# Optimization experiments

Measured on AMD Instinct MI355X. Metric: run time of the kernel, lower is better.

The kernel has to match this reference:

```python
import jax, jax.numpy as jnp
import numpy as np

B, N, M = 8, 1024, 64          # graphs, ops/graph, machines/graph
OPF, MF = 16, 8                # raw feature dims
H, D, L = 8, 64, 3             # heads, head dim, HGT layers
F = H * D                      # 512 = hidden_dim * num_heads
KC = 8                         # compatible machines per op
NOP, NM = B * N, B * M
EPS = 1e-5


def _graph_ln(x, w, b):
    # PyG LayerNorm(mode='graph') with batch=None: scalar mean/std over the whole tensor
    x = x - x.mean()
    return x / (x.std() + EPS) * w + b


def _seg_softmax(a, idx, n):
    amax = jax.ops.segment_max(a, idx, num_segments=n)
    amax = jnp.where(jnp.isfinite(amax), amax, 0.0)
    ex = jnp.exp(a - amax[idx])
    s = jax.ops.segment_sum(ex, idx, num_segments=n)
    return ex / (s[idx] + 1e-16)


def _forward(op_x, machine_x, W_emb_op, b_emb_op, W_emb_m, b_emb_m,
             opn_w, opn_b, mn_w, mn_b, Wk, bk, Wq, bq, Wv, bv,
             A_rel, M_rel, p_rel, W_out, b_out, skip, ln_w, ln_b,
             ei_precedes, ei_canproc, ei_compat):
    x_op = _graph_ln(op_x @ W_emb_op + b_emb_op, opn_w, opn_b)
    x_m = _graph_ln(machine_x @ W_emb_m + b_emb_m, mn_w, mn_b)
    s0, d0 = ei_precedes   # op -> op
    s1, d1 = ei_canproc    # machine -> op
    s2, d2 = ei_compat     # op -> machine
    scale = 1.0 / jnp.sqrt(jnp.float32(D))
    for l in range(L):
        k_op = (x_op @ Wk[l, 0] + bk[l, 0]).reshape(NOP, H, D)
        q_op = (x_op @ Wq[l, 0] + bq[l, 0]).reshape(NOP, H, D)
        v_op = (x_op @ Wv[l, 0] + bv[l, 0]).reshape(NOP, H, D)
        k_m = (x_m @ Wk[l, 1] + bk[l, 1]).reshape(NM, H, D)
        q_m = (x_m @ Wq[l, 1] + bq[l, 1]).reshape(NM, H, D)
        v_m = (x_m @ Wv[l, 1] + bv[l, 1]).reshape(NM, H, D)
        # relation-specific per-head transforms (a_rel/m_rel of HGTConv)
        k0 = jnp.einsum('nhd,hde->nhe', k_op, A_rel[l, 0]); v0 = jnp.einsum('nhd,hde->nhe', v_op, M_rel[l, 0])
        k1 = jnp.einsum('nhd,hde->nhe', k_m, A_rel[l, 1]);  v1 = jnp.einsum('nhd,hde->nhe', v_m, M_rel[l, 1])
        k2 = jnp.einsum('nhd,hde->nhe', k_op, A_rel[l, 2]); v2 = jnp.einsum('nhd,hde->nhe', v_op, M_rel[l, 2])
        # attention into op nodes: joint softmax over both incoming edge types
        a0 = (q_op[d0] * k0[s0]).sum(-1) * p_rel[l, 0] * scale   # [E0,H]
        a1 = (q_op[d1] * k1[s1]).sum(-1) * p_rel[l, 1] * scale   # [E1,H]
        a_op = jnp.concatenate([a0, a1]); dd = jnp.concatenate([d0, d1])
        w = _seg_softmax(a_op, dd, NOP)
        msg = jnp.concatenate([v0[s0], v1[s1]]) * w[:, :, None]
        agg_op = jax.ops.segment_sum(msg, dd, num_segments=NOP).reshape(NOP, F)
        # attention into machine nodes
        a2 = (q_m[d2] * k2[s2]).sum(-1) * p_rel[l, 2] * scale
        w2 = _seg_softmax(a2, d2, NM)
        agg_m = jax.ops.segment_sum(v2[s2] * w2[:, :, None], d2, num_segments=NM).reshape(NM, F)
        # output projection + learned skip gate (HGTConv internals)
        o_op = jax.nn.gelu(agg_op, approximate=False) @ W_out[l, 0] + b_out[l, 0]
        o_m = jax.nn.gelu(agg_m, approximate=False) @ W_out[l, 1] + b_out[l, 1]
        g_op = jax.nn.sigmoid(skip[l, 0]); g_m = jax.nn.sigmoid(skip[l, 1])
        o_op = g_op * o_op + (1.0 - g_op) * x_op
        o_m = g_m * o_m + (1.0 - g_m) * x_m
        # wrapper residual + dropout(eval=identity) + graph layer norm
        x_op = _graph_ln(o_op + x_op, ln_w[l], ln_b[l])
        x_m = _graph_ln(o_m + x_m, ln_w[l], ln_b[l])
    fea_j = x_op.reshape(B, N, F)
    fea_m = x_m.reshape(B, M, F)
    return fea_j, fea_m, fea_j.mean(1, keepdims=True), fea_m.mean(1, keepdims=True)


def setup_inputs() -> dict:
    key = jax.random.key(0)
    ks = jax.random.split(key, 12)
    rng = np.random.default_rng(0)
    ids = np.arange(NOP).reshape(B, N)
    src0 = ids[:, :-1].ravel(); dst0 = ids[:, 1:].ravel()
    mach = rng.integers(0, M, size=(B, N, KC)) + (np.arange(B) * M)[:, None, None]
    ops = np.broadcast_to(ids[:, :, None], (B, N, KC))
    ei_precedes = jnp.asarray(np.stack([src0, dst0]), dtype=jnp.int32)
    ei_canproc = jnp.asarray(np.stack([mach.ravel(), ops.ravel()]), dtype=jnp.int32)
    ei_compat = jnp.asarray(np.stack([ops.ravel(), mach.ravel()]), dtype=jnp.int32)
    n = lambda k, sh, s=0.05: jax.random.normal(k, sh, dtype=jnp.float32) * s
    return dict(
        op_x=n(ks[0], (NOP, OPF), 1.0),
        machine_x=n(ks[1], (NM, MF), 1.0),
        W_emb_op=n(ks[2], (OPF, F)), b_emb_op=jnp.zeros((F,), jnp.float32),
        W_emb_m=n(ks[3], (MF, F)), b_emb_m=jnp.zeros((F,), jnp.float32),
        opn_w=jnp.ones((F,), jnp.float32), opn_b=jnp.zeros((F,), jnp.float32),
        mn_w=jnp.ones((F,), jnp.float32), mn_b=jnp.zeros((F,), jnp.float32),
        Wk=n(ks[4], (L, 2, F, F)), bk=jnp.zeros((L, 2, F), jnp.float32),
        Wq=n(ks[5], (L, 2, F, F)), bq=jnp.zeros((L, 2, F), jnp.float32),
        Wv=n(ks[6], (L, 2, F, F)), bv=jnp.zeros((L, 2, F), jnp.float32),
        A_rel=n(ks[7], (L, 3, H, D, D)), M_rel=n(ks[8], (L, 3, H, D, D)),
        p_rel=jnp.ones((L, 3, H), jnp.float32),
        W_out=n(ks[9], (L, 2, F, F)), b_out=jnp.zeros((L, 2, F), jnp.float32),
        skip=jnp.ones((L, 2), jnp.float32),
        ln_w=jnp.ones((L, F), jnp.float32), ln_b=jnp.zeros((L, F), jnp.float32),
        ei_precedes=ei_precedes, ei_canproc=ei_canproc, ei_compat=ei_compat,
    )


def reference(op_x, machine_x, W_emb_op, b_emb_op, W_emb_m, b_emb_m,
              opn_w, opn_b, mn_w, mn_b, Wk, bk, Wq, bq, Wv, bv,
              A_rel, M_rel, p_rel, W_out, b_out, skip, ln_w, ln_b,
              ei_precedes, ei_canproc, ei_compat):
    return _forward(op_x, machine_x, W_emb_op, b_emb_op, W_emb_m, b_emb_m,
                    opn_w, opn_b, mn_w, mn_b, Wk, bk, Wq, bq, Wv, bv,
                    A_rel, M_rel, p_rel, W_out, b_out, skip, ln_w, ln_b,
                    ei_precedes, ei_canproc, ei_compat)
```

## Files before the change

kernel.cpp:

```cpp
#include <hip/hip_runtime.h>

typedef unsigned short u16;
typedef __attribute__((ext_vector_type(4))) float floatx4;
typedef __attribute__((ext_vector_type(8))) short shortx8;
typedef __attribute__((ext_vector_type(4))) short shortx4;

#define NOPS 8192
#define NMS  512
#define CQ   2560
#define CM   1536
#define TOPC (NOPS*512)
#define TMC  (NMS*512)

__device__ __forceinline__ float bf2f(u16 u){ return __uint_as_float(((unsigned)u)<<16); }
__device__ __forceinline__ u16 f2bf(float f){
  unsigned u = __float_as_uint(f);
  u += 0x7FFFu + ((u>>16)&1u);
  return (u16)(u>>16);
}
__device__ __forceinline__ float wred(float v){
  #pragma unroll
  for (int o=32;o;o>>=1) v += __shfl_xor(v,o,64);
  return v;
}
__device__ __forceinline__ float geluf(float x){
  return 0.5f*x*(1.f+erff(x*0.70710678118654752f));
}
__device__ __forceinline__ void block_stat_out2(float s, float s2, float* pstat, int slot){
  __shared__ float sb[8];
  s = wred(s); s2 = wred(s2);
  int wv = threadIdx.x >> 6;
  if ((threadIdx.x & 63) == 0){ sb[wv*2] = s; sb[wv*2+1] = s2; }
  __syncthreads();
  if (threadIdx.x == 0){
    float a = 0.f, b = 0.f;
    int nw = blockDim.x >> 6;
    for (int i=0;i<nw;++i){ a += sb[i*2]; b += sb[i*2+1]; }
    pstat[slot*2]   = a;
    pstat[slot*2+1] = b;
  }
}

__global__ __launch_bounds__(256) void setup_all_k(
    const int* __restrict__ s1, float* __restrict__ Ct, float* __restrict__ Cn,
    const float* __restrict__ bq, float* bias_op, float* bias_m,
    const float* __restrict__ bk, const float* __restrict__ bv,
    const float* __restrict__ Ar, const float* __restrict__ Mr,
    const float* __restrict__ Wout, const float* __restrict__ Wq,
    u16* __restrict__ Wout_t, u16* __restrict__ Wc_op_t, u16* __restrict__ Wc_m_t,
    const float* __restrict__ Wk, const float* __restrict__ Wv,
    const float* __restrict__ Xop, const float* __restrict__ Wop, const float* __restrict__ bop,
    float* __restrict__ Yop, u16* __restrict__ Yop_bf,
    const float* __restrict__ Xm, const float* __restrict__ Wm, const float* __restrict__ bm_,
    float* __restrict__ Ym, u16* __restrict__ Ym_bf,
    float* pstat, float* pstat_m){
  __shared__ __align__(16) char smem[27648];
  int bid = blockIdx.x;
  int tid = threadIdx.x;
  if (bid < 2048){
    int idx = bid*256 + tid;
    int n = idx >> 6, l = idx & 63;
    const int* row = s1 + n*8;
    int cnt = 0;
    #pragma unroll
    for (int j=0;j<8;++j) cnt += ((row[j] & 63) == l);
    float f = (float)cnt;
    Cn[(size_t)n*64 + l] = f;
    int b = n >> 10, nl = n & 1023;
    Ct[(size_t)((b<<6) + l)*1024 + nl] = f;
  } else if (bid < 2060){
    int i = (bid-2048)*256 + tid;
    int l = i >> 10, side = (i >> 9) & 1, f = i & 511;
    float v = bq[(l*2+side)*512 + f];
    if (side==0) bias_op[l*CQ + f] = v; else bias_m[l*CM + f] = v;
  } else if (bid < 2204){
    if (tid >= 64) return;
    int gx = bid - 2060; int e = tid;
    int l = gx/48; int rem = gx - l*48; int s = rem >> 3; int h = rem & 7;
    int side = (s < 4) ? 0 : 1;
    int r = (s < 4) ? (s+1) : (s-3);
    int useK = side==0 ? (s==0 || s==2) : (s==4);
    int rel  = side==0 ? ((s<2)?0:2) : 1;
    const float* bb  = (useK ? bk : bv) + (size_t)(l*2+side)*512 + h*64;
    const float* Rel = (useK ? Ar : Mr) + ((size_t)(l*3+rel)*8 + h)*4096;
    float acc = 0.f;
    for (int d=0; d<64; ++d) acc += bb[d]*Rel[d*64 + e];
    float* bias = side ? (bias_m + l*CM) : (bias_op + l*CQ);
    bias[r*512 + h*64 + e] = acc;
  } else if (bid < 2972){
    u16 (*t)[65] = (u16(*)[65])smem;
    int id2 = bid - 2204;
    int g = id2 >> 6; int rem = id2 & 63;
    int kb = (rem >> 3) * 64, nb = (rem & 7) * 64;
    const float* s; u16* d;
    if (g < 6){
      s = Wout + (size_t)g*262144;
      d = Wout_t + (size_t)g*262144;
    } else {
      int blk = g - 6; int l = blk >> 1, side = blk & 1;
      s = Wq + (size_t)blk*262144;
      d = side ? (Wc_m_t + (size_t)l*CM*512) : (Wc_op_t + (size_t)l*CQ*512);
    }
    int tx = tid & 63, ty4 = tid >> 6;
    #pragma unroll 4
    for (int p=0;p<16;++p){
      int k = ty4 + p*4;
      t[k][tx] = f2bf(s[(size_t)(kb+k)*512 + nb + tx]);
    }
    __syncthreads();
    #pragma unroll 4
    for (int p=0;p<16;++p){
      int n = ty4 + p*4;
      d[(size_t)(nb+n)*512 + kb + tx] = t[tx][n];
    }
  } else if (bid < 3548){
    u16* As = (u16*)smem;
    u16* Bs = As + 64*72;
    int id3 = bid - 2972;
    int gx = id3 >> 2;
    int cc0 = (id3 & 3) * 128;
    int l = gx/48; int rem = gx - l*48; int s = rem >> 3; int h = rem & 7;
    int side = (s < 4) ? 0 : 1;
    int r = (s < 4) ? (s+1) : (s-3);
    int useK = side==0 ? (s==0 || s==2) : (s==4);
    int rel  = side==0 ? ((s<2)?0:2) : 1;
    const float* W   = (useK ? Wk : Wv) + (size_t)(l*2+side)*262144;
    const float* Rel = (useK ? Ar : Mr) + ((size_t)(l*3+rel)*8 + h)*4096;
    int h64 = h*64;
    u16* Wt = side ? (Wc_m_t + (size_t)l*CM*512) : (Wc_op_t + (size_t)l*CQ*512);
    int rbase = r*512 + h64;
    int lane = tid & 63, wave = tid >> 6;
    {
      int d = tid >> 2, e0 = (tid & 3) * 16;
      #pragma unroll
      for (int j=0;j<16;++j) As[(e0+j)*72 + d] = f2bf(Rel[d*64 + e0 + j]);
    }
    {
      int ccl = tid >> 1, d0 = (tid & 1) * 32;
      const float* src = W + (size_t)(cc0+ccl)*512 + h64 + d0;
      #pragma unroll
      for (int j=0;j<32;j+=4){
        floatx4 v = *(const floatx4*)(src + j);
        shortx4 sv;
        #pragma unroll
        for (int e=0;e<4;++e) sv[e] = (short)f2bf(v[e]);
        *(shortx4*)(Bs + ccl*72 + d0 + j) = sv;
      }
    }
    __syncthreads();
    int wm = wave & 1, wn = wave >> 1;
    int mrow = lane & 15, quad = lane >> 4;
    floatx4 acc[2][4];
    #pragma unroll
    for (int a=0;a<2;++a)
      #pragma unroll
      for (int b=0;b<4;++b) acc[a][b] = (floatx4){0.f,0.f,0.f,0.f};
    #pragma unroll
    for (int ks=0; ks<2; ++ks){
      shortx8 af[2], bf[4];
      #pragma unroll
      for (int mt=0;mt<2;++mt) af[mt] = *(const shortx8*)(As + (wm*32 + mt*16 + mrow)*72 + ks*32 + quad*8);
      #pragma unroll
      for (int nt=0;nt<4;++nt) bf[nt] = *(const shortx8*)(Bs + (wn*64 + nt*16 + mrow)*72 + ks*32 + quad*8);
      #pragma unroll
      for (int mt=0;mt<2;++mt)
        #pragma unroll
        for (int nt=0;nt<4;++nt)
          acc[mt][nt] = __builtin_amdgcn_mfma_f32_16x16x32_bf16(af[mt], bf[nt], acc[mt][nt], 0, 0, 0);
    }
    #pragma unroll
    for (int mt=0;mt<2;++mt){
      #pragma unroll
      for (int nt=0;nt<4;++nt){
        int ccl = wn*64 + nt*16 + mrow;
        #pragma unroll
        for (int r2=0;r2<4;++r2){
          int e = wm*32 + mt*16 + quad*4 + r2;
          Wt[(size_t)(rbase + e)*512 + cc0 + ccl] = f2bf(acc[mt][nt][r2]);
        }
      }
    }
  } else {
    int eb = bid - 3548;
    const float *X, *W, *bias; float *Y, *ps; u16* Yb; int K, total, nb, lb;
    if (eb < 1024){ X=Xop; W=Wop; bias=bop; Y=Yop; Yb=Yop_bf; ps=pstat;   K=16; total=TOPC; nb=1024; lb=eb; }
    else          { X=Xm;  W=Wm;  bias=bm_; Y=Ym;  Yb=Ym_bf;  ps=pstat_m; K=8;  total=TMC;  nb=128;  lb=eb-1024; }
    float s = 0.f, s2 = 0.f;
    for (int idx = lb*256 + tid; idx < total; idx += nb*256){
      int n = idx >> 9, f = idx & 511;
      float v = bias[f];
      for (int c=0;c<K;++c) v += X[n*K+c] * W[c*512+f];
      Y[idx] = v;
      Yb[idx] = f2bf(v);
      s += v; s2 += v*v;
    }
    block_stat_out2(s, s2, ps, lb);
  }
}

__global__ __launch_bounds__(256) void foldk(u16* __restrict__ Wc_op_t, u16* __restrict__ Wc_m_t,
                                             float* __restrict__ bias_op, float* __restrict__ bias_m,
                                             float* __restrict__ u_op, float* __restrict__ u_m,
                                             const float* __restrict__ opn_w, const float* __restrict__ opn_b,
                                             const float* __restrict__ mn_w, const float* __restrict__ mn_b,
                                             const float* __restrict__ ln_w, const float* __restrict__ ln_b){
  int bid = blockIdx.x, tid = threadIdx.x;
  int rloc = tid >> 2, t = tid & 3;
  int side, l; u16* Wt; float* bias; float* u;
  if (bid < 120){
    int row = bid*64 + rloc; side = 0; l = row/2560; int j = row - l*2560;
    Wt = Wc_op_t + ((size_t)l*CQ + j)*512; bias = bias_op + l*CQ + j; u = u_op + l*CQ + j;
  } else {
    int row = (bid-120)*64 + rloc; side = 1; l = row/1536; int j = row - l*1536;
    Wt = Wc_m_t + ((size_t)l*CM + j)*512; bias = bias_m + l*CM + j; u = u_m + l*CM + j;
  }
  const float* w = side ? (l==0 ? mn_w : ln_w + (l-1)*512) : (l==0 ? opn_w : ln_w + (l-1)*512);
  const float* b = side ? (l==0 ? mn_b : ln_b + (l-1)*512) : (l==0 ? opn_b : ln_b + (l-1)*512);
  float up = 0.f, vp = 0.f;
  for (int k = t*128; k < t*128 + 128; k += 8){
    shortx8 wv = *(shortx8*)(Wt + k);
    #pragma unroll
    for (int e=0;e<8;++e){
      float x = bf2f((u16)wv[e]);
      float wk = w[k+e];
      up += wk*x; vp += b[k+e]*x;
      wv[e] = (short)f2bf(x*wk);
    }
    *(shortx8*)(Wt + k) = wv;
  }
  up += __shfl_xor(up,1,64); up += __shfl_xor(up,2,64);
  vp += __shfl_xor(vp,1,64); vp += __shfl_xor(vp,2,64);
  if (t == 0){ *u = up; *bias += vp; }
}

__global__ __launch_bounds__(256) void ln2_k(const float* __restrict__ src_op, float* __restrict__ dst_op,
                                             const float* __restrict__ w_op, const float* __restrict__ b_op,
                                             const float* __restrict__ src_m, float* __restrict__ dst_m,
                                             const float* __restrict__ w_m, const float* __restrict__ b_m,
                                             const float* __restrict__ pstat, const float* __restrict__ pstat_m,
                                             int nbo, int nbm){
  int bid = blockIdx.x;
  const float *src, *w, *b, *ps; float* dst; int total4, nb, lb, nblk; float inv_n;
  if (bid < 1024){ src=src_op; dst=dst_op; w=w_op; b=b_op; ps=pstat;
                   total4=TOPC/4; nb=1024; lb=bid; nblk=nbo; inv_n=1.f/TOPC; }
  else           { src=src_m;  dst=dst_m;  w=w_m;  b=b_m;  ps=pstat_m;
                   total4=TMC/4;  nb=128;  lb=bid-1024; nblk=nbm; inv_n=1.f/TMC; }
  __shared__ float sb[8];
  __shared__ float mr[2];
  float s = 0.f, s2 = 0.f;
  for (int i = threadIdx.x; i < nblk; i += 256){ s += ps[2*i]; s2 += ps[2*i+1]; }
  s = wred(s); s2 = wred(s2);
  int wv = threadIdx.x >> 6;
  if ((threadIdx.x & 63) == 0){ sb[wv*2] = s; sb[wv*2+1] = s2; }
  __syncthreads();
  if (threadIdx.x == 0){
    float a = 0.f, bsum = 0.f;
    for (int i=0;i<4;++i){ a += sb[i*2]; bsum += sb[i*2+1]; }
    float mean = a * inv_n;
    float var  = fmaxf(bsum * inv_n - mean*mean, 0.f);
    mr[0] = mean;
    mr[1] = 1.f/(sqrtf(var) + 1e-5f);
  }
  __syncthreads();
  float mean = mr[0], rinv = mr[1];
  const floatx4* s4 = (const floatx4*)src;
  floatx4* d4 = (floatx4*)dst;
  const floatx4* w4 = (const floatx4*)w;
  const floatx4* b4 = (const floatx4*)b;
  for (int i = lb*256 + threadIdx.x; i < total4; i += nb*256){
    int f = i & 127;
    floatx4 v = s4[i], wv2 = w4[f], bv = b4[f];
    #pragma unroll
    for (int e=0;e<4;++e) v[e] = (v[e]-mean)*rinv*wv2[e] + bv[e];
    d4[i] = v;
  }
}

__device__ __forceinline__ void gemm_gate_core(u16* As, u16* Bs, float* stb,
                                               const u16* __restrict__ A, const u16* __restrict__ Bt,
                                               const float* __restrict__ xr, const float* __restrict__ bo,
                                               const float* __restrict__ sk,
                                               const float* __restrict__ lnw, const float* __restrict__ lnb,
                                               const float* __restrict__ psr, int np, float inv_n,
                                               float* __restrict__ Y, u16* __restrict__ Ybf,
                                               float* pstat, int slot, int bx, int by){
  const int tid = threadIdx.x;
  const int lane = tid & 63, wave = tid >> 6;
  {
    float s = 0.f, s2 = 0.f;
    for (int i = tid; i < np; i += 256){ s += psr[2*i]; s2 += psr[2*i+1]; }
    s = wred(s); s2 = wred(s2);
    if (lane == 0){ stb[wave*2] = s; stb[wave*2+1] = s2; }
    __syncthreads();
    if (tid == 0){
      float a = 0.f, bb = 0.f;
      for (int i=0;i<4;++i){ a += stb[2*i]; bb += stb[2*i+1]; }
      float mean = a * inv_n;
      float var = fmaxf(bb * inv_n - mean*mean, 0.f);
      stb[8] = mean;
      stb[9] = 1.f/(sqrtf(var) + 1e-5f);
    }
    __syncthreads();
  }
  const float mean = stb[8], rinv = stb[9];
  const int bm = by * 128, bn = bx * 128;
  const int wm = wave & 1, wn = wave >> 1;
  const int mrow = lane & 15, quad = lane >> 4;
  const u16* Ab = A + (size_t)bm*512;
  const u16* Bb = Bt + (size_t)bn*512;
  floatx4 acc[4][4];
  #pragma unroll
  for (int a=0;a<4;++a)
    #pragma unroll
    for (int b=0;b<4;++b) acc[a][b] = (floatx4){0.f,0.f,0.f,0.f};
  const int r0 = tid >> 2, c0 = (tid & 3) * 8;
  const int r1 = (tid+256) >> 2, c1 = ((tid+256) & 3) * 8;
  const int lds0 = wave*512;
  const int lds1 = wave*512 + 2048;
  for (int k0 = 0; k0 < 512; k0 += 32){
    __builtin_amdgcn_global_load_lds((const __attribute__((address_space(1))) void*)(Ab + (size_t)r0*512 + k0 + c0),
                                     (__attribute__((address_space(3))) void*)(As + lds0), 16, 0, 0);
    __builtin_amdgcn_global_load_lds((const __attribute__((address_space(1))) void*)(Ab + (size_t)r1*512 + k0 + c1),
                                     (__attribute__((address_space(3))) void*)(As + lds1), 16, 0, 0);
    __builtin_amdgcn_global_load_lds((const __attribute__((address_space(1))) void*)(Bb + (size_t)r0*512 + k0 + c0),
                                     (__attribute__((address_space(3))) void*)(Bs + lds0), 16, 0, 0);
    __builtin_amdgcn_global_load_lds((const __attribute__((address_space(1))) void*)(Bb + (size_t)r1*512 + k0 + c1),
                                     (__attribute__((address_space(3))) void*)(Bs + lds1), 16, 0, 0);
    __syncthreads();
    shortx8 af[4], bf[4];
    #pragma unroll
    for (int mt=0;mt<4;++mt) af[mt] = *(const shortx8*)(As + (wm*64 + mt*16 + mrow)*32 + quad*8);
    #pragma unroll
    for (int nt=0;nt<4;++nt) bf[nt] = *(const shortx8*)(Bs + (wn*64 + nt*16 + mrow)*32 + quad*8);
    #pragma unroll
    for (int mt=0;mt<4;++mt)
      #pragma unroll
      for (int nt=0;nt<4;++nt)
        acc[mt][nt] = __builtin_amdgcn_mfma_f32_16x16x32_bf16(af[mt], bf[nt], acc[mt][nt], 0, 0, 0);
    __syncthreads();
  }
  float g = 1.f/(1.f+expf(-(*sk)));
  float s = 0.f, s2 = 0.f;
  #pragma unroll
  for (int mt=0;mt<4;++mt){
    #pragma unroll
    for (int nt=0;nt<4;++nt){
      int col = bn + wn*64 + nt*16 + mrow;
      float bval = bo[col];
      float lw = lnw[col]*rinv, lb = lnb[col];
      #pragma unroll
      for (int r2=0;r2<4;++r2){
        int row = bm + wm*64 + mt*16 + quad*4 + r2;
        float v = acc[mt][nt][r2] + bval;
        float xv = (xr[(size_t)row*512 + col] - mean)*lw + lb;
        float o = g*v + (2.f-g)*xv;
        Y[(size_t)row*512 + col] = o;
        Ybf[(size_t)row*512 + col] = f2bf(o);
        s += o; s2 += o*o;
      }
    }
  }
  block_stat_out2(s, s2, pstat, slot);
}
__global__ __launch_bounds__(256) void gemmgate2_k(
    const u16* A1, const u16* B1, const float* x1, const float* bo1, const float* sk1,
    const float* lnw1, const float* lnb1, float* Y1, u16* Yb1, float* ps1w, int nblk1,
    const u16* A2, const u16* B2, const float* x2, const float* bo2, const float* sk2,
    const float* lnw2, const float* lnb2, float* Y2, u16* Yb2, float* ps2w,
    const float* ps1r, int np1, const float* ps2r, int np2){
  __shared__ u16 As[128*32];
  __shared__ u16 Bs[128*32];
  __shared__ float stb[12];
  int id = blockIdx.x;
  if (id < nblk1)
    gemm_gate_core(As, Bs, stb, A1, B1, x1, bo1, sk1, lnw1, lnb1, ps1r, np1, 1.f/TOPC,
                   Y1, Yb1, ps1w, id, id % 4, id / 4);
  else {
    int j = id - nblk1;
    gemm_gate_core(As, Bs, stb, A2, B2, x2, bo2, sk2, lnw2, lnb2, ps2r, np2, 1.f/TMC,
                   Y2, Yb2, ps2w, j, j % 4, j / 4);
  }
}

__device__ __forceinline__ void stage_half8(const u16* __restrict__ src, int kc, u16* region, int tid){
  int wave = tid >> 6;
  #pragma unroll
  for (int j=0;j<2;++j){
    int idx = j*512 + tid;
    int row = idx >> 2, qp2 = idx & 3;
    int qs = qp2 ^ (((row >> 3) & 1) << 1);
    __builtin_amdgcn_global_load_lds(
      (const __attribute__((address_space(1))) void*)(src + (size_t)row*512 + kc + qs*8),
      (__attribute__((address_space(3))) void*)(region + (j*512 + wave*64)*8),
      16, 0, 0);
  }
}

#define MFMA_QUAD(MH) do { \
  __builtin_amdgcn_s_barrier(); \
  asm volatile("s_waitcnt lgkmcnt(0)" ::: "memory"); \
  __builtin_amdgcn_sched_barrier(0); \
  __builtin_amdgcn_s_setprio(1); \
  _Pragma("unroll") \
  for (int mt=0;mt<4;++mt){ \
    _Pragma("unroll") \
    for (int nt=0;nt<4;++nt) \
      acc[(MH)*4+mt][nt] = __builtin_amdgcn_mfma_f32_16x16x32_bf16(af[mt], bf[nt], acc[(MH)*4+mt][nt], 0, 0, 0); \
  } \
  __builtin_amdgcn_s_setprio(0); \
} while(0)

__global__ __launch_bounds__(512, 2) void gemm8_k(
    const u16* __restrict__ A1, const u16* __restrict__ B1, const float* __restrict__ bias1,
    const float* __restrict__ u1, u16* __restrict__ C1, int N1, int nbx1, int nblk1,
    const u16* __restrict__ A2, const u16* __restrict__ B2, const float* __restrict__ bias2p,
    const float* __restrict__ u2, u16* __restrict__ C2, int N2, int nbx2,
    const float* __restrict__ ps1, int np1, const float* __restrict__ ps2, int np2){
  extern __shared__ u16 lds[];
  float* statsh = (float*)(lds + 65536);
  int id = blockIdx.x;
  const u16 *A, *Bt; const float *bias, *uvec, *ps; u16* C; int N, bx, by, np; float inv_n;
  if (id < nblk1){
    int xcd = id & 7, loc = id >> 3;
    int wg = xcd * (nblk1 >> 3) + loc;
    A=A1; Bt=B1; bias=bias1; uvec=u1; C=C1; N=N1; bx=wg%nbx1; by=wg/nbx1;
    ps=ps1; np=np1; inv_n=1.f/TOPC;
  }
  else { int j=id-nblk1; A=A2; Bt=B2; bias=bias2p; uvec=u2; C=C2; N=N2; bx=j%nbx2; by=j/nbx2;
    ps=ps2; np=np2; inv_n=1.f/TMC; }
  const int tid = threadIdx.x, lane = tid & 63, wave = tid >> 6;
  {
    float s = 0.f, s2 = 0.f;
    for (int i = tid; i < np; i += 512){ s += ps[2*i]; s2 += ps[2*i+1]; }
    s = wred(s); s2 = wred(s2);
    if (lane == 0){ statsh[wave*2] = s; statsh[wave*2+1] = s2; }
    __syncthreads();
    if (tid == 0){
      float a = 0.f, bb = 0.f;
      for (int i=0;i<8;++i){ a += statsh[2*i]; bb += statsh[2*i+1]; }
      float mean = a * inv_n;
      float var = fmaxf(bb * inv_n - mean*mean, 0.f);
      statsh[16] = mean;
      statsh[17] = 1.f/(sqrtf(var) + 1e-5f);
    }
    __syncthreads();
  }
  const float mean = statsh[16], rinv = statsh[17];
  const int wm = wave & 1, wn = wave >> 1;
  const int mrow = lane & 15, quad = lane >> 4;
  const int qp = quad ^ ((mrow & 8) ? 2 : 0);
  const u16* Ab = A + (size_t)(by*256)*512;
  const u16* Bb = Bt + (size_t)(bx*256)*512;

  floatx4 acc[8][4];
  #pragma unroll
  for (int a=0;a<8;++a)
    #pragma unroll
    for (int b=0;b<4;++b) acc[a][b] = (floatx4){0.f,0.f,0.f,0.f};

  stage_half8(Ab, 0,  lds,          tid);
  stage_half8(Bb, 0,  lds + 16384,  tid);
  stage_half8(Ab, 32, lds + 8192,   tid);
  stage_half8(Bb, 32, lds + 24576,  tid);
  stage_half8(Ab, 64, lds + 32768,  tid);
  stage_half8(Bb, 64, lds + 49152,  tid);
  asm volatile("s_waitcnt vmcnt(8)" ::: "memory");
  __builtin_amdgcn_s_barrier();

  for (int t = 0; t < 8; ++t){
    const int s = t & 1;
    u16* Sbase = lds + s*32768;
    u16* Obase = lds + (s^1)*32768;
    const u16* a0 = Sbase + (wm*128 + mrow)*32 + qp*8;
    const u16* b0 = Sbase + 16384 + (wn*64 + mrow)*32 + qp*8;
    const int kc1 = ((t < 7) ? (t+1) : 7)*64 + 32;
    const int kc2 = ((t < 6) ? (t+2) : 7)*64;
    shortx8 af[4], bf[4];

    #pragma unroll
    for (int mt=0;mt<4;++mt) af[mt] = *(const shortx8*)(a0 + mt*512);
    #pragma unroll
    for (int nt=0;nt<4;++nt) bf[nt] = *(const shortx8*)(b0 + nt*512);
    stage_half8(Ab, kc1, Obase + 8192, tid);
    MFMA_QUAD(0);
    __builtin_amdgcn_s_barrier();

    #pragma unroll
    for (int mt=0;mt<4;++mt) af[mt] = *(const shortx8*)(a0 + 2048 + mt*512);
    stage_half8(Bb, kc1, Obase + 24576, tid);
    MFMA_QUAD(1);
    asm volatile("s_waitcnt vmcnt(8)" ::: "memory");
    __builtin_amdgcn_s_barrier();

    #pragma unroll
    for (int mt=0;mt<4;++mt) af[mt] = *(const shortx8*)(a0 + 8192 + mt*512);
    #pragma unroll
    for (int nt=0;nt<4;++nt) bf[nt] = *(const shortx8*)(b0 + 8192 + nt*512);
    stage_half8(Ab, kc2, Sbase, tid);
    MFMA_QUAD(0);
    __builtin_amdgcn_s_barrier();

    #pragma unroll
    for (int mt=0;mt<4;++mt) af[mt] = *(const shortx8*)(a0 + 8192 + 2048 + mt*512);
    stage_half8(Bb, kc2, Sbase + 16384, tid);
    MFMA_QUAD(1);
    asm volatile("s_waitcnt vmcnt(8)" ::: "memory");
    __builtin_amdgcn_s_barrier();
  }

  const float rm = rinv*mean;
  const int crow0 = by*256 + wm*128 + quad*4;
  const int ccol0 = bx*256 + wn*64 + mrow;
  float bv[4], uv[4];
  #pragma unroll
  for (int nt=0;nt<4;++nt){
    int col = ccol0 + nt*16;
    bv[nt] = bias[col];
    uv[nt] = uvec[col];
  }
  #pragma unroll
  for (int mh=0;mh<2;++mh){
    #pragma unroll
    for (int mt=0;mt<4;++mt){
      int row = crow0 + mh*64 + mt*16;
      #pragma unroll
      for (int nt=0;nt<4;++nt){
        int col = ccol0 + nt*16;
        #pragma unroll
        for (int r2=0;r2<4;++r2)
          C[(size_t)(row+r2)*N + col] = f2bf(rinv*acc[mh*4+mt][nt][r2] + bv[nt] - rm*uv[nt]);
      }
    }
  }
}

__global__ __launch_bounds__(256) void attn_k(const u16* __restrict__ qkv_op, const u16* __restrict__ qkv_m,
                                              const float* __restrict__ prel, const float* __restrict__ Cn,
                                              const float* __restrict__ Ct,
                                              u16* __restrict__ agg_op, u16* __restrict__ agg_m){
  __shared__ __align__(16) char smem[43520];
  int id = blockIdx.x;
  int tid = threadIdx.x, lane = tid & 63, wave = tid >> 6;
  int mrow = lane & 15, quad = lane >> 4;
  if (id < 1024){
    u16* smem16 = (u16*)smem;
    u16* As = smem16;
    u16* Bs = smem16 + 4608;
    float* Sbuf = (float*)smem;
    u16* P   = smem16 + 9216;
    u16* v1T = smem16 + 13824;
    float* wpreS = (float*)(smem + 36864);
    float* linvS = (float*)(smem + 37120);
    int bh = id >> 4; int b = bh >> 3, h = bh & 7;
    int n0 = (id & 15) * 64;
    int wm = wave & 1, wn = wave >> 1;
    int srow = tid >> 2, scol = (tid & 3) * 16;
    float p1 = prel[8 + h] * 0.125f;
    {
      const u16* src = qkv_op + (size_t)(b*1024 + n0 + srow)*CQ + h*64 + scol;
      *(shortx8*)(As + srow*72 + scol)     = *(const shortx8*)(src);
      *(shortx8*)(As + srow*72 + scol + 8) = *(const shortx8*)(src + 8);
    }
    {
      const u16* src = qkv_m + (size_t)(b*64 + srow)*CM + 512 + h*64 + scol;
      *(shortx8*)(Bs + srow*72 + scol)     = *(const shortx8*)(src);
      *(shortx8*)(Bs + srow*72 + scol + 8) = *(const shortx8*)(src + 8);
    }
    {
      const u16* src = qkv_m + (size_t)(b*64 + srow)*CM + 1024 + h*64 + scol;
      shortx8 v0 = *(const shortx8*)(src);
      shortx8 v1 = *(const shortx8*)(src + 8);
      #pragma unroll
      for (int e=0;e<8;++e){ v1T[(scol+e)*72 + srow] = (u16)v0[e]; v1T[(scol+8+e)*72 + srow] = (u16)v1[e]; }
    }
    __syncthreads();
    floatx4 acc[2][2];
    #pragma unroll
    for (int a=0;a<2;++a){ acc[a][0] = (floatx4){0,0,0,0}; acc[a][1] = (floatx4){0,0,0,0}; }
    #pragma unroll
    for (int ks=0; ks<2; ++ks){
      shortx8 af[2], bf[2];
      #pragma unroll
      for (int mt=0;mt<2;++mt) af[mt] = *(const shortx8*)(As + (wm*32 + mt*16 + mrow)*72 + ks*32 + quad*8);
      #pragma unroll
      for (int nt=0;nt<2;++nt) bf[nt] = *(const shortx8*)(Bs + (wn*32 + nt*16 + mrow)*72 + ks*32 + quad*8);
      #pragma unroll
      for (int mt=0;mt<2;++mt)
        #pragma unroll
        for (int nt=0;nt<2;++nt)
          acc[mt][nt] = __builtin_amdgcn_mfma_f32_16x16x32_bf16(af[mt], bf[nt], acc[mt][nt], 0, 0, 0);
    }
    __syncthreads();
    #pragma unroll
    for (int mt=0;mt<2;++mt){
      #pragma unroll
      for (int nt=0;nt<2;++nt){
        int m = wn*32 + nt*16 + mrow;
        #pragma unroll
        for (int r2=0;r2<4;++r2){
          int nl = wm*32 + mt*16 + quad*4 + r2;
          Sbuf[nl*66 + m] = acc[mt][nt][r2] * p1;
        }
      }
    }
    __syncthreads();
    {
      int row = srow;
      int mb  = scol;
      int n_g = b*1024 + n0 + row;
      int nl  = n0 + row;
      float sp = -1e30f;
      if (nl > 0){
        float p0 = prel[h] * 0.125f;
        const u16* qp = qkv_op + (size_t)n_g*CQ + h*64 + mb;
        const u16* kp = qkv_op + (size_t)(n_g-1)*CQ + 512 + h*64 + mb;
        shortx8 qa = *(const shortx8*)(qp), qb2 = *(const shortx8*)(qp + 8);
        shortx8 ka = *(const shortx8*)(kp), kb2 = *(const shortx8*)(kp + 8);
        float d = 0.f;
        #pragma unroll
        for (int e=0;e<8;++e) d += bf2f((u16)qa[e])*bf2f((u16)ka[e]) + bf2f((u16)qb2[e])*bf2f((u16)kb2[e]);
        d += __shfl_xor(d, 1, 64);
        d += __shfl_xor(d, 2, 64);
        sp = d * p0;
      }
      const float* crow = Cn + (size_t)n_g*64 + mb;
      float cv[16];
      float mx = sp;
      #pragma unroll
      for (int j=0;j<16;++j){
        cv[j] = crow[j];
        if (cv[j] > 0.f) mx = fmaxf(mx, Sbuf[row*66 + mb + j]);
      }
      mx = fmaxf(mx, __shfl_xor(mx, 1, 64));
      mx = fmaxf(mx, __shfl_xor(mx, 2, 64));
      float L = 0.f;
      #pragma unroll
      for (int j=0;j<16;j+=4){
        shortx4 pv;
        #pragma unroll
        for (int e=0;e<4;++e){
          float w = (cv[j+e] > 0.f) ? cv[j+e]*expf(Sbuf[row*66 + mb + j + e] - mx) : 0.f;
          L += w;
          pv[e] = (short)f2bf(w);
        }
        *(shortx4*)(P + row*72 + mb + j) = pv;
      }
      L += __shfl_xor(L, 1, 64);
      L += __shfl_xor(L, 2, 64);
      float ep = (nl > 0) ? expf(sp - mx) : 0.f;
      L += ep;
      if ((tid & 3) == 0){ wpreS[row] = ep; linvS[row] = 1.f/(L + 1e-16f); }
    }
    __syncthreads();
    floatx4 po[2][2];
    #pragma unroll
    for (int a=0;a<2;++a){ po[a][0] = (floatx4){0,0,0,0}; po[a][1] = (floatx4){0,0,0,0}; }
    #pragma unroll
    for (int ks=0; ks<2; ++ks){
      shortx8 paf[2], pbf[2];
      #pragma unroll
      for (int mt=0;mt<2;++mt) paf[mt] = *(const shortx8*)(P + (wm*32 + mt*16 + mrow)*72 + ks*32 + quad*8);
      #pragma unroll
      for (int nt=0;nt<2;++nt) pbf[nt] = *(const shortx8*)(v1T + (wn*32 + nt*16 + mrow)*72 + ks*32 + quad*8);
      #pragma unroll
      for (int mt=0;mt<2;++mt)
        #pragma unroll
        for (int nt=0;nt<2;++nt)
          po[mt][nt] = __builtin_amdgcn_mfma_f32_16x16x32_bf16(paf[mt], pbf[nt], po[mt][nt], 0, 0, 0);
    }
    #pragma unroll
    for (int mt=0;mt<2;++mt){
      #pragma unroll
      for (int nt=0;nt<2;++nt){
        int d = wn*32 + nt*16 + mrow;
        #pragma unroll
        for (int r2=0;r2<4;++r2){
          int rl = wm*32 + mt*16 + quad*4 + r2;
          int n = n0 + rl;
          size_t ng = (size_t)b*1024 + n;
          float v = po[mt][nt][r2];
          if (n > 0) v += wpreS[rl] * bf2f(qkv_op[(ng-1)*CQ + 1024 + h*64 + d]);
          v *= linvS[rl];
          agg_op[ng*512 + h*64 + d] = f2bf(geluf(v));
        }
      }
    }
  } else {
    u16* qs  = (u16*)smem;
    u16* ks  = (u16*)(smem + 2304);
    u16* vsT = (u16*)(smem + 20736);
    u16* Ps  = (u16*)(smem + 38144);
    float (*redv)[4][16] = (float(*)[4][16])(smem + 42496);
    int id2 = id - 1024;
    int g = id2 & 3; int bh = id2 >> 2; int b = bh >> 3, h = bh & 7;
    int w = wave;
    float p2 = prel[16 + h] * 0.125f;
    if (tid < 128){
      int r = tid >> 3, cg = (tid & 7) * 8;
      *(shortx8*)(qs + r*72 + cg) = *(const shortx8*)(qkv_m + (size_t)(b*64 + g*16 + r)*CM + h*64 + cg);
    }
    const float* ctbase = Ct + (size_t)(b*64 + g*16 + mrow)*1024;
    float mx = -1e30f;
    for (int ch = 0; ch < 8; ++ch){
      int nb = ch*128;
      #pragma unroll
      for (int i=0;i<4;++i){
        int idx = i*256 + tid;
        int r = idx >> 3, cg = (idx & 7) * 8;
        *(shortx8*)(ks + r*72 + cg) =
          *(const shortx8*)(qkv_op + (size_t)(b*1024 + nb + r)*CQ + 1536 + h*64 + cg);
      }
      __syncthreads();
      #pragma unroll
      for (int nt=0; nt<2; ++nt){
        floatx4 acc = (floatx4){0,0,0,0};
        #pragma unroll
        for (int kk=0; kk<2; ++kk){
          shortx8 af = *(const shortx8*)(ks + (w*32 + nt*16 + mrow)*72 + kk*32 + quad*8);
          shortx8 bf = *(const shortx8*)(qs + mrow*72 + kk*32 + quad*8);
          acc = __builtin_amdgcn_mfma_f32_16x16x32_bf16(af, bf, acc, 0, 0, 0);
        }
        int nloc = w*32 + nt*16 + quad*4;
        floatx4 cv = *(const floatx4*)(ctbase + nb + nloc);
        #pragma unroll
        for (int r2=0;r2<4;++r2)
          if (cv[r2] > 0.f) mx = fmaxf(mx, acc[r2]*p2);
      }
      __syncthreads();
    }
    mx = fmaxf(mx, __shfl_xor(mx, 16, 64));
    mx = fmaxf(mx, __shfl_xor(mx, 32, 64));
    if (lane < 16) redv[0][w][lane] = mx;
    __syncthreads();
    mx = fmaxf(fmaxf(redv[0][0][mrow], redv[0][1][mrow]), fmaxf(redv[0][2][mrow], redv[0][3][mrow]));
    float L = 0.f;
    floatx4 O = (floatx4){0,0,0,0};
    for (int ch = 0; ch < 8; ++ch){
      int nb = ch*128;
      #pragma unroll
      for (int i=0;i<4;++i){
        int idx = i*256 + tid;
        int r = idx >> 3, cg = (idx & 7) * 8;
        *(shortx8*)(ks + r*72 + cg) =
          *(const shortx8*)(qkv_op + (size_t)(b*1024 + nb + r)*CQ + 1536 + h*64 + cg);
        shortx8 vv = *(const shortx8*)(qkv_op + (size_t)(b*1024 + nb + r)*CQ + 2048 + h*64 + cg);
        #pragma unroll
        for (int e=0;e<8;++e) vsT[(cg+e)*136 + r] = (u16)vv[e];
      }
      __syncthreads();
      #pragma unroll
      for (int nt=0; nt<2; ++nt){
        floatx4 acc = (floatx4){0,0,0,0};
        #pragma unroll
        for (int kk=0; kk<2; ++kk){
          shortx8 af = *(const shortx8*)(ks + (w*32 + nt*16 + mrow)*72 + kk*32 + quad*8);
          shortx8 bf = *(const shortx8*)(qs + mrow*72 + kk*32 + quad*8);
          acc = __builtin_amdgcn_mfma_f32_16x16x32_bf16(af, bf, acc, 0, 0, 0);
        }
        int nloc = w*32 + nt*16 + quad*4;
        floatx4 cv = *(const floatx4*)(ctbase + nb + nloc);
        shortx4 pv;
        #pragma unroll
        for (int r2=0;r2<4;++r2){
          float e = (cv[r2] > 0.f) ? cv[r2]*expf(acc[r2]*p2 - mx) : 0.f;
          L += e;
          pv[r2] = (short)f2bf(e);
        }
        *(shortx4*)(Ps + mrow*136 + nloc) = pv;
      }
      __syncthreads();
      #pragma unroll
      for (int kk=0; kk<4; ++kk){
        shortx8 af = *(const shortx8*)(Ps + mrow*136 + kk*32 + quad*8);
        shortx8 bf = *(const shortx8*)(vsT + (w*16 + mrow)*136 + kk*32 + quad*8);
        O = __builtin_amdgcn_mfma_f32_16x16x32_bf16(af, bf, O, 0, 0, 0);
      }
      __syncthreads();
    }
    L += __shfl_xor(L, 16, 64);
    L += __shfl_xor(L, 32, 64);
    if (lane < 16) redv[1][w][lane] = L;
    __syncthreads();
    #pragma unroll
    for (int r2=0;r2<4;++r2){
      int m = quad*4 + r2;
      float Ls = redv[1][0][m] + redv[1][1][m] + redv[1][2][m] + redv[1][3][m];
      float v = O[r2] / (Ls + 1e-16f);
      agg_m[(size_t)(b*64 + g*16 + m)*512 + h*64 + w*16 + mrow] = f2bf(geluf(v));
    }
  }
}

__global__ __launch_bounds__(512) void meanj_part_k(const float* __restrict__ xo, float* scratchJ){
  int b = blockIdx.x, chunk = blockIdx.y, f = threadIdx.x;
  float s = 0.f;
  for (int r=0;r<128;++r){
    int row = b*1024 + chunk*128 + r;
    s += xo[(size_t)row*512 + f];
  }
  scratchJ[(b*8 + chunk)*512 + f] = s;
}
__global__ __launch_bounds__(512) void mean2_k(const float* __restrict__ scratchJ, float* __restrict__ out){
  int i = blockIdx.x*512 + threadIdx.x;
  if (i < 4096){
    int b = i >> 9, f = i & 511;
    float s = 0.f;
    #pragma unroll
    for (int c=0;c<8;++c) s += scratchJ[(b*8+c)*512 + f];
    out[4456448 + i] = s * (1.f/1024.f);
  } else {
    int j = i - 4096;
    int b = j >> 9, f = j & 511;
    float s = 0.f;
    for (int r=0;r<64;++r) s += out[(size_t)TOPC + (size_t)(b*64+r)*512 + f];
    out[4460544 + j] = s * (1.f/64.f);
  }
}

extern "C" void kernel_launch(void* const* d_in, const int* in_sizes, int n_in,
                              void* d_out, int out_size, void* d_ws, size_t ws_size,
                              hipStream_t stream){
  const float* op_x      = (const float*)d_in[0];
  const float* machine_x = (const float*)d_in[1];
  const float* W_emb_op  = (const float*)d_in[2];
  const float* b_emb_op  = (const float*)d_in[3];
  const float* W_emb_m   = (const float*)d_in[4];
  const float* b_emb_m   = (const float*)d_in[5];
  const float* opn_w     = (const float*)d_in[6];
  const float* opn_b     = (const float*)d_in[7];
  const float* mn_w      = (const float*)d_in[8];
  const float* mn_b      = (const float*)d_in[9];
  const float* Wk        = (const float*)d_in[10];
  const float* bk        = (const float*)d_in[11];
  const float* Wq        = (const float*)d_in[12];
  const float* bq        = (const float*)d_in[13];
  const float* Wv        = (const float*)d_in[14];
  const float* bv        = (const float*)d_in[15];
  const float* A_rel     = (const float*)d_in[16];
  const float* M_rel     = (const float*)d_in[17];
  const float* p_rel     = (const float*)d_in[18];
  const float* W_out     = (const float*)d_in[19];
  const float* b_out     = (const float*)d_in[20];
  const float* skip      = (const float*)d_in[21];
  const float* ln_w      = (const float*)d_in[22];
  const float* ln_b      = (const float*)d_in[23];
  const int* s1          = (const int*)d_in[25];
  float* out = (float*)d_out;

  char* ws = (char*)d_ws;
  size_t off = 0;
  auto alloc = [&](size_t bytes)->void*{
    void* p = ws + off;
    off = (off + bytes + 255) & ~(size_t)255;
    return p;
  };
  float* pstat     = (float*)alloc(8192*4);
  float* scratchJ  = (float*)alloc(32768*4);
  float* Ct        = (float*)alloc((size_t)NMS*1024*4);
  float* Cn        = (float*)alloc((size_t)NOPS*64*4);
  float* x_op      = (float*)alloc((size_t)NOPS*512*4);
  u16*   x_op_bf   = (u16*)  alloc((size_t)NOPS*512*2);
  float* x_m       = (float*)alloc((size_t)NMS*512*4);
  u16*   x_m_bf    = (u16*)  alloc((size_t)NMS*512*2);
  u16*   qkv_op    = (u16*)  alloc((size_t)NOPS*CQ*2);
  u16*   qkv_m     = (u16*)  alloc((size_t)NMS*CM*2);
  u16*   agg_op    = (u16*)  alloc((size_t)NOPS*512*2);
  u16*   agg_m     = (u16*)  alloc((size_t)NMS*512*2);
  u16*   Wc_op_t   = (u16*)  alloc((size_t)3*CQ*512*2);
  float* bias_op   = (float*)alloc((size_t)3*CQ*4);
  u16*   Wc_m_t    = (u16*)  alloc((size_t)3*CM*512*2);
  float* bias_m    = (float*)alloc((size_t)3*CM*4);
  float* u_op      = (float*)alloc((size_t)3*CQ*4);
  float* u_m       = (float*)alloc((size_t)3*CM*4);
  u16*   Wout_t    = (u16*)  alloc((size_t)6*262144*2);
  float* psA   = pstat;          float* psA_m = pstat + 2048;
  float* psB   = pstat + 4096;   float* psB_m = pstat + 6144;

  setup_all_k<<<4700,256,0,stream>>>(s1, Ct, Cn, bq, bias_op, bias_m, bk, bv, A_rel, M_rel,
                                     W_out, Wq, Wout_t, Wc_op_t, Wc_m_t, Wk, Wv,
                                     op_x, W_emb_op, b_emb_op, x_op, x_op_bf,
                                     machine_x, W_emb_m, b_emb_m, x_m, x_m_bf, psA, psA_m);
  foldk<<<192,256,0,stream>>>(Wc_op_t, Wc_m_t, bias_op, bias_m, u_op, u_m,
                              opn_w, opn_b, mn_w, mn_b, ln_w, ln_b);

  for (int l=0; l<3; ++l){
    float *psR, *psR_m, *psW, *psW_m; int npo, npm;
    if (l == 0){ psR=psA; psR_m=psA_m; psW=psB; psW_m=psB_m; npo=1024; npm=128; }
    else if (l == 1){ psR=psB; psR_m=psB_m; psW=psA; psW_m=psA_m; npo=256; npm=16; }
    else { psR=psA; psR_m=psA_m; psW=psB; psW_m=psB_m; npo=256; npm=16; }
    const float* lnw_o = (l==0) ? opn_w : ln_w + (l-1)*512;
    const float* lnb_o = (l==0) ? opn_b : ln_b + (l-1)*512;
    const float* lnw_m2 = (l==0) ? mn_w : ln_w + (l-1)*512;
    const float* lnb_m2 = (l==0) ? mn_b : ln_b + (l-1)*512;
    gemm8_k<<<332,512,131136,stream>>>(x_op_bf, Wc_op_t + (size_t)l*CQ*512, bias_op + l*CQ, u_op + l*CQ,
                                       qkv_op, CQ, 10, 320,
                                       x_m_bf, Wc_m_t + (size_t)l*CM*512, bias_m + l*CM, u_m + l*CM,
                                       qkv_m, CM, 6,
                                       psR, npo, psR_m, npm);
    attn_k<<<1280,256,0,stream>>>(qkv_op, qkv_m, p_rel + l*24, Cn, Ct, agg_op, agg_m);
    gemmgate2_k<<<272,256,0,stream>>>(agg_op, Wout_t + (size_t)(l*2+0)*262144, x_op,
                                      b_out + (size_t)(l*2+0)*512, skip + l*2+0,
                                      lnw_o, lnb_o, x_op, x_op_bf, psW, 256,
                                      agg_m, Wout_t + (size_t)(l*2+1)*262144, x_m,
                                      b_out + (size_t)(l*2+1)*512, skip + l*2+1,
                                      lnw_m2, lnb_m2, x_m, x_m_bf, psW_m,
                                      psR, npo, psR_m, npm);
  }

  ln2_k<<<1152,256,0,stream>>>(x_op, out, ln_w + 1024, ln_b + 1024,
                               x_m, out + TOPC, ln_w + 1024, ln_b + 1024,
                               psB, psB_m, 256, 16);

  meanj_part_k<<<dim3(8,8),512,0,stream>>>(out, scratchJ);
  mean2_k<<<16,512,0,stream>>>(scratchJ, out);
}
```

Measured before the change: 588.4 us.

## Use online softmax for machine attention and schedule those blocks first

The machine-side attention blocks previously made two passes over all op keys, one to find the row max and one to compute exp and accumulate P·V. They now use a single-pass online softmax that rescales L and O as the running max changes, so K is loaded only once. These longer-running blocks are also moved to the lowest block ids so they launch first and do not trail behind the op-side blocks. The cost is an extra barrier and a cross-wave max reduction in every chunk.

```diff
diff --git a/kernel.cpp b/kernel.cpp
--- a/kernel.cpp
+++ b/kernel.cpp
@@ -542,7 +542,115 @@
   int id = blockIdx.x;
   int tid = threadIdx.x, lane = tid & 63, wave = tid >> 6;
   int mrow = lane & 15, quad = lane >> 4;
-  if (id < 1024){
+  if (id < 256){
+    u16* qs  = (u16*)smem;
+    u16* ks  = (u16*)(smem + 2304);
+    u16* vsT = (u16*)(smem + 20736);
+    u16* Ps  = (u16*)(smem + 38144);
+    float (*redv)[4][16] = (float(*)[4][16])(smem + 42496);
+    int g = id & 3; int bh = id >> 2; int b = bh >> 3, h = bh & 7;
+    int w = wave;
+    float p2 = prel[16 + h] * 0.125f;
+    if (tid < 128){
+      int r = tid >> 3, cg = (tid & 7) * 8;
+      *(shortx8*)(qs + r*72 + cg) = *(const shortx8*)(qkv_m + (size_t)(b*64 + g*16 + r)*CM + h*64 + cg);
+    }
+    const float* ctbase = Ct + (size_t)(b*64 + g*16 + mrow)*1024;
+    float mold_m = -1e30f;
+    float mold4[4] = {-1e30f,-1e30f,-1e30f,-1e30f};
+    float L = 0.f;
+    floatx4 O = (floatx4){0,0,0,0};
+    for (int ch = 0; ch < 8; ++ch){
+      int nb = ch*128;
+      #pragma unroll
+      for (int i=0;i<4;++i){
+        int idx = i*256 + tid;
+        int r = idx >> 3, cg = (idx & 7) * 8;
+        *(shortx8*)(ks + r*72 + cg) =
+          *(const shortx8*)(qkv_op + (size_t)(b*1024 + nb + r)*CQ + 1536 + h*64 + cg);
+        shortx8 vv = *(const shortx8*)(qkv_op + (size_t)(b*1024 + nb + r)*CQ + 2048 + h*64 + cg);
+        #pragma unroll
+        for (int e=0;e<8;++e) vsT[(cg+e)*136 + r] = (u16)vv[e];
+      }
+      __syncthreads();
+      floatx4 sa[2], cv[2];
+      #pragma unroll
+      for (int nt=0; nt<2; ++nt){
+        floatx4 acc = (floatx4){0,0,0,0};
+        #pragma unroll
+        for (int kk=0; kk<2; ++kk){
+          shortx8 af = *(const shortx8*)(ks + (w*32 + nt*16 + mrow)*72 + kk*32 + quad*8);
+          shortx8 bf = *(const shortx8*)(qs + mrow*72 + kk*32 + quad*8);
+          acc = __builtin_amdgcn_mfma_f32_16x16x32_bf16(af, bf, acc, 0, 0, 0);
+        }
+        int nloc = w*32 + nt*16 + quad*4;
+        cv[nt] = *(const floatx4*)(ctbase + nb + nloc);
+        #pragma unroll
+        for (int r2=0;r2<4;++r2) acc[r2] *= p2;
+        sa[nt] = acc;
+      }
+      float cm = -1e30f;
+      #pragma unroll
+      for (int nt=0;nt<2;++nt)
+        #pragma unroll
+        for (int r2=0;r2<4;++r2)
+          if (cv[nt][r2] > 0.f) cm = fmaxf(cm, sa[nt][r2]);
+      cm = fmaxf(cm, __shfl_xor(cm, 16, 64));
+      cm = fmaxf(cm, __shfl_xor(cm, 32, 64));
+      if (lane < 16) redv[0][w][lane] = cm;
+      __syncthreads();
+      float mnew_m = fmaxf(fmaxf(redv[0][0][mrow], redv[0][1][mrow]),
+                           fmaxf(redv[0][2][mrow], redv[0][3][mrow]));
+      mnew_m = fmaxf(mnew_m, mold_m);
+      float sL = expf(mold_m - mnew_m);
+      mold_m = mnew_m;
+      float sO[4];
+      #pragma unroll
+      for (int r2=0;r2<4;++r2){
+        int r = quad*4 + r2;
+        float mn = fmaxf(fmaxf(redv[0][0][r], redv[0][1][r]),
+                         fmaxf(redv[0][2][r], redv[0][3][r]));
+        mn = fmaxf(mn, mold4[r2]);
+        sO[r2] = expf(mold4[r2] - mn);
+        mold4[r2] = mn;
+      }
+      float Lsum = 0.f;
+      #pragma unroll
+      for (int nt=0;nt<2;++nt){
+        int nloc = w*32 + nt*16 + quad*4;
+        shortx4 pv;
+        #pragma unroll
+        for (int r2=0;r2<4;++r2){
+          float e = (cv[nt][r2] > 0.f) ? cv[nt][r2]*expf(sa[nt][r2] - mnew_m) : 0.f;
+          Lsum += e;
+          pv[r2] = (short)f2bf(e);
+        }
+        *(shortx4*)(Ps + mrow*136 + nloc) = pv;
+      }
+      L = L*sL + Lsum;
+      __syncthreads();
+      #pragma unroll
+      for (int r2=0;r2<4;++r2) O[r2] *= sO[r2];
+      #pragma unroll
+      for (int kk=0; kk<4; ++kk){
+        shortx8 af = *(const shortx8*)(Ps + mrow*136 + kk*32 + quad*8);
+        shortx8 bf = *(const shortx8*)(vsT + (w*16 + mrow)*136 + kk*32 + quad*8);
+        O = __builtin_amdgcn_mfma_f32_16x16x32_bf16(af, bf, O, 0, 0, 0);
+      }
+      __syncthreads();
+    }
+    L += __shfl_xor(L, 16, 64);
+    L += __shfl_xor(L, 32, 64);
+    if (lane < 16) redv[1][w][lane] = L;
+    __syncthreads();
+    #pragma unroll
+    for (int r2=0;r2<4;++r2){
+      int m = quad*4 + r2;
+      float Ls = redv[1][0][m] + redv[1][1][m] + redv[1][2][m] + redv[1][3][m];
+      float v = O[r2] / (Ls + 1e-16f);
+      agg_m[(size_t)(b*64 + g*16 + m)*512 + h*64 + w*16 + mrow] = f2bf(geluf(v));
+    }
+  } else {
     u16* smem16 = (u16*)smem;
     u16* As = smem16;
     u16* Bs = smem16 + 4608;
@@ -551,8 +659,9 @@
     u16* v1T = smem16 + 13824;
     float* wpreS = (float*)(smem + 36864);
     float* linvS = (float*)(smem + 37120);
-    int bh = id >> 4; int b = bh >> 3, h = bh & 7;
-    int n0 = (id & 15) * 64;
+    int id2 = id - 256;
+    int bh = id2 >> 4; int b = bh >> 3, h = bh & 7;
+    int n0 = (id2 & 15) * 64;
     int wm = wave & 1, wn = wave >> 1;
     int srow = tid >> 2, scol = (tid & 3) * 16;
     float p1 = prel[8 + h] * 0.125f;
@@ -684,109 +793,6 @@
           agg_op[ng*512 + h*64 + d] = f2bf(geluf(v));
         }
       }
-    }
-  } else {
-    u16* qs  = (u16*)smem;
-    u16* ks  = (u16*)(smem + 2304);
-    u16* vsT = (u16*)(smem + 20736);
-    u16* Ps  = (u16*)(smem + 38144);
-    float (*redv)[4][16] = (float(*)[4][16])(smem + 42496);
-    int id2 = id - 1024;
-    int g = id2 & 3; int bh = id2 >> 2; int b = bh >> 3, h = bh & 7;
-    int w = wave;
-    float p2 = prel[16 + h] * 0.125f;
-    if (tid < 128){
-      int r = tid >> 3, cg = (tid & 7) * 8;
-      *(shortx8*)(qs + r*72 + cg) = *(const shortx8*)(qkv_m + (size_t)(b*64 + g*16 + r)*CM + h*64 + cg);
-    }
-    const float* ctbase = Ct + (size_t)(b*64 + g*16 + mrow)*1024;
-    float mx = -1e30f;
-    for (int ch = 0; ch < 8; ++ch){
-      int nb = ch*128;
-      #pragma unroll
-      for (int i=0;i<4;++i){
-        int idx = i*256 + tid;
-        int r = idx >> 3, cg = (idx & 7) * 8;
-        *(shortx8*)(ks + r*72 + cg) =
-          *(const shortx8*)(qkv_op + (size_t)(b*1024 + nb + r)*CQ + 1536 + h*64 + cg);
-      }
-      __syncthreads();
-      #pragma unroll
-      for (int nt=0; nt<2; ++nt){
-        floatx4 acc = (floatx4){0,0,0,0};
-        #pragma unroll
-        for (int kk=0; kk<2; ++kk){
-          shortx8 af = *(const shortx8*)(ks + (w*32 + nt*16 + mrow)*72 + kk*32 + quad*8);
-          shortx8 bf = *(const shortx8*)(qs + mrow*72 + kk*32 + quad*8);
-          acc = __builtin_amdgcn_mfma_f32_16x16x32_bf16(af, bf, acc, 0, 0, 0);
-        }
-        int nloc = w*32 + nt*16 + quad*4;
-        floatx4 cv = *(const floatx4*)(ctbase + nb + nloc);
-        #pragma unroll
-        for (int r2=0;r2<4;++r2)
-          if (cv[r2] > 0.f) mx = fmaxf(mx, acc[r2]*p2);
-      }
-      __syncthreads();
-    }
-    mx = fmaxf(mx, __shfl_xor(mx, 16, 64));
-    mx = fmaxf(mx, __shfl_xor(mx, 32, 64));
-    if (lane < 16) redv[0][w][lane] = mx;
-    __syncthreads();
-    mx = fmaxf(fmaxf(redv[0][0][mrow], redv[0][1][mrow]), fmaxf(redv[0][2][mrow], redv[0][3][mrow]));
-    float L = 0.f;
-    floatx4 O = (floatx4){0,0,0,0};
-    for (int ch = 0; ch < 8; ++ch){
-      int nb = ch*128;
-      #pragma unroll
-      for (int i=0;i<4;++i){
-        int idx = i*256 + tid;
-        int r = idx >> 3, cg = (idx & 7) * 8;
-        *(shortx8*)(ks + r*72 + cg) =
-          *(const shortx8*)(qkv_op + (size_t)(b*1024 + nb + r)*CQ + 1536 + h*64 + cg);
-        shortx8 vv = *(const shortx8*)(qkv_op + (size_t)(b*1024 + nb + r)*CQ + 2048 + h*64 + cg);
-        #pragma unroll
-        for (int e=0;e<8;++e) vsT[(cg+e)*136 + r] = (u16)vv[e];
-      }
-      __syncthreads();
-      #pragma unroll
-      for (int nt=0; nt<2; ++nt){
-        floatx4 acc = (floatx4){0,0,0,0};
-        #pragma unroll
-        for (int kk=0; kk<2; ++kk){
-          shortx8 af = *(const shortx8*)(ks + (w*32 + nt*16 + mrow)*72 + kk*32 + quad*8);
-          shortx8 bf = *(const shortx8*)(qs + mrow*72 + kk*32 + quad*8);
-          acc = __builtin_amdgcn_mfma_f32_16x16x32_bf16(af, bf, acc, 0, 0, 0);
-        }
-        int nloc = w*32 + nt*16 + quad*4;
-        floatx4 cv = *(const floatx4*)(ctbase + nb + nloc);
-        shortx4 pv;
-        #pragma unroll
-        for (int r2=0;r2<4;++r2){
-          float e = (cv[r2] > 0.f) ? cv[r2]*expf(acc[r2]*p2 - mx) : 0.f;
-          L += e;
-          pv[r2] = (short)f2bf(e);
-        }
-        *(shortx4*)(Ps + mrow*136 + nloc) = pv;
-      }
-      __syncthreads();
-      #pragma unroll
-      for (int kk=0; kk<4; ++kk){
-        shortx8 af = *(const shortx8*)(Ps + mrow*136 + kk*32 + quad*8);
-        shortx8 bf = *(const shortx8*)(vsT + (w*16 + mrow)*136 + kk*32 + quad*8);
-        O = __builtin_amdgcn_mfma_f32_16x16x32_bf16(af, bf, O, 0, 0, 0);
-      }
-      __syncthreads();
-    }
-    L += __shfl_xor(L, 16, 64);
-    L += __shfl_xor(L, 32, 64);
-    if (lane < 16) redv[1][w][lane] = L;
-    __syncthreads();
-    #pragma unroll
-    for (int r2=0;r2<4;++r2){
-      int m = quad*4 + r2;
-      float Ls = redv[1][0][m] + redv[1][1][m] + redv[1][2][m] + redv[1][3][m];
-      float v = O[r2] / (Ls + 1e-16f);
-      agg_m[(size_t)(b*64 + g*16 + m)*512 + h*64 + w*16 + mrow] = f2bf(geluf(v));
     }
   }
 }
```

New measurement: 525.0 us. 10.8% less time.
